# Kernel tuning notes

Hardware: AMD Instinct MI355X
Metric: run time of the kernel (lower is better)

The kernel has to match this reference:

```python
import jax, jax.numpy as jnp
import numpy as np

HEAD_SIZE = 128
NEG_INF = -1000000000.0

def setup_inputs() -> dict:
    key = jax.random.key(0)
    k1, k2, k3, k4 = jax.random.split(key, 4)
    B, T, C = 8, 2048, 1024
    x = jax.random.normal(k1, (B, T, C), dtype=jnp.float32)
    Wq = jax.random.normal(k2, (C, HEAD_SIZE), dtype=jnp.float32) * (1.0 / np.sqrt(C))
    Wk = jax.random.normal(k3, (C, HEAD_SIZE), dtype=jnp.float32) * (1.0 / np.sqrt(C))
    Wv = jax.random.normal(k4, (C, HEAD_SIZE), dtype=jnp.float32) * (1.0 / np.sqrt(C))
    return {"x": x, "Wq": Wq, "Wk": Wk, "Wv": Wv}

def reference(x, Wq, Wk, Wv):
    # x: [B, T, C]; projections: [B, T, H]
    T = x.shape[1]
    q = jnp.einsum('btc,ch->bth', x, Wq)
    k = jnp.einsum('btc,ch->bth', x, Wk)
    v = jnp.einsum('btc,ch->bth', x, Wv)
    scale = 1.0 / jnp.sqrt(jnp.float32(HEAD_SIZE))
    wei = jnp.einsum('bth,bsh->bts', q, k) * scale  # [B, T, T]
    causal = jnp.tril(jnp.ones((T, T), dtype=bool))
    wei = jnp.where(causal, wei, NEG_INF)
    wei = jax.nn.softmax(wei, axis=-1)
    # dropout is identity (deterministic=True)
    out = jnp.einsum('bts,bsh->bth', wei, v)  # [B, T, H]
    return out
```

## Files before the change

### kernel.cpp

```cpp
#include <hip/hip_runtime.h>
#include <hip/hip_bf16.h>
#include <stdint.h>

#define B_ 8
#define T_ 2048
#define C_ 1024
#define H_ 128
#define BT (B_*T_)
#define SCALE 0.08838834764831845f
#define SCL2  0.12751949703928947f
#define MFIX2 28.853900817779268f
#define CH 4
#define SLOTS_PB 140

typedef __attribute__((ext_vector_type(8))) short bf16x8;
typedef __attribute__((ext_vector_type(4))) float f32x4;

__device__ __forceinline__ ushort f2bf(float f) {
  union { float f; uint32_t u; } un; un.f = f;
  return (ushort)((un.u + 0x7fffu + ((un.u >> 16) & 1u)) >> 16);
}
__device__ __forceinline__ ushort f2bf_t(float f) {
  union { float f; uint32_t u; } un; un.f = f;
  return (ushort)(un.u >> 16);
}
__device__ __forceinline__ float bf2f(ushort h) {
  union { uint32_t u; float f; } un; un.u = ((uint32_t)h) << 16;
  return un.f;
}
__device__ __forceinline__ void gload16(const void* g, void* l) {
  __builtin_amdgcn_global_load_lds(
      (const __attribute__((address_space(1))) void*)g,
      (__attribute__((address_space(3))) void*)l, 16, 0, 0);
}

__global__ __launch_bounds__(256) void wtrans_kernel(
    const float* __restrict__ Wq, const float* __restrict__ Wk,
    const float* __restrict__ Wv, ushort* __restrict__ wt)
{
  const int tt = blockIdx.x * 256 + threadIdx.x;
  const int n = tt >> 6;
  const int k0 = (tt & 63) << 4;
  const float* W = (n < 128) ? Wq : (n < 256 ? Wk : Wv);
  const int h = n & 127;
  ushort tmp[16];
  #pragma unroll
  for (int j = 0; j < 16; ++j)
    tmp[j] = f2bf(W[(size_t)(k0 + j) * H_ + h]);
  *reinterpret_cast<bf16x8*>(&wt[(size_t)n * C_ + k0]) =
      *reinterpret_cast<bf16x8*>(&tmp[0]);
  *reinterpret_cast<bf16x8*>(&wt[(size_t)n * C_ + k0 + 8]) =
      *reinterpret_cast<bf16x8*>(&tmp[8]);
}

__global__ __launch_bounds__(256, 3) void proj_kernel(
    const float* __restrict__ x, const ushort* __restrict__ wt,
    ushort* __restrict__ qh, ushort* __restrict__ kh, ushort* __restrict__ vt)
{
  __shared__ __align__(16) ushort As[64][128];
  __shared__ __align__(16) ushort Bs[128][128];
  const int tid  = threadIdx.x;
  const int lane = tid & 63, wave = tid >> 6;
  const int l15  = lane & 15, l4 = lane >> 4;
  const int o  = (blockIdx.x & 7) * 96 + (blockIdx.x >> 3);
  const int mb = o / 3, nb = o - mb * 3;
  const int m0 = mb * 64, n0 = nb * 128;
  const int wr = wave >> 1, wc = wave & 1;

  f32x4 acc[2][4];
  #pragma unroll
  for (int i = 0; i < 2; ++i)
    #pragma unroll
    for (int j = 0; j < 4; ++j) acc[i][j] = f32x4{0.f, 0.f, 0.f, 0.f};

  for (int k0 = 0; k0 < C_; k0 += 128) {
    __syncthreads();
    #pragma unroll
    for (int j = 0; j < 8; ++j) {
      const int seg = wave * 8 + j;
      const int r = seg * 4 + (lane >> 4);
      const int c8 = lane & 15;
      const int c8g = (c8 & 8) | ((c8 & 7) ^ (r & 7));
      gload16(&wt[(size_t)(n0 + r) * C_ + k0 + c8g * 8], &Bs[seg * 4][0]);
    }
    float4 av[8];
    #pragma unroll
    for (int it = 0; it < 8; ++it) {
      const int f4 = it * 256 + tid;
      const int r = f4 >> 5, c4 = f4 & 31;
      av[it] = *reinterpret_cast<const float4*>(
          &x[(size_t)(m0 + r) * C_ + k0 + 4 * c4]);
    }
    #pragma unroll
    for (int it = 0; it < 8; ++it) {
      const int f4 = it * 256 + tid;
      const int r = f4 >> 5, c4 = f4 & 31;
      ushort4 pk;
      pk.x = f2bf(av[it].x); pk.y = f2bf(av[it].y);
      pk.z = f2bf(av[it].z); pk.w = f2bf(av[it].w);
      const int c = c4 >> 1;
      const int pos = (c & 8) | ((c & 7) ^ (r & 7));
      *reinterpret_cast<ushort4*>(&As[r][pos * 8 + (c4 & 1) * 4]) = pk;
    }
    __syncthreads();

    #pragma unroll
    for (int kv = 0; kv < 2; ++kv) {
      bf16x8 a[2][2], b[4][2];
      #pragma unroll
      for (int mi = 0; mi < 2; ++mi)
        #pragma unroll
        for (int kc = 0; kc < 2; ++kc) {
          const int row = wr * 32 + mi * 16 + l15;
          const int kc4 = (kv * 2 + kc) * 4 + l4;
          const int pos = (kc4 & 8) | ((kc4 & 7) ^ (row & 7));
          a[mi][kc] = *reinterpret_cast<const bf16x8*>(&As[row][pos * 8]);
        }
      #pragma unroll
      for (int ni = 0; ni < 4; ++ni)
        #pragma unroll
        for (int kc = 0; kc < 2; ++kc) {
          const int row = wc * 64 + ni * 16 + l15;
          const int kc4 = (kv * 2 + kc) * 4 + l4;
          const int pos = (kc4 & 8) | ((kc4 & 7) ^ (row & 7));
          b[ni][kc] = *reinterpret_cast<const bf16x8*>(&Bs[row][pos * 8]);
        }
      __builtin_amdgcn_s_setprio(1);
      if (nb != 2) {
        #pragma unroll
        for (int mi = 0; mi < 2; ++mi)
          #pragma unroll
          for (int ni = 0; ni < 4; ++ni)
            #pragma unroll
            for (int kc = 0; kc < 2; ++kc)
              acc[mi][ni] = __builtin_amdgcn_mfma_f32_16x16x32_bf16(
                  a[mi][kc], b[ni][kc], acc[mi][ni], 0, 0, 0);
      } else {
        #pragma unroll
        for (int mi = 0; mi < 2; ++mi)
          #pragma unroll
          for (int ni = 0; ni < 4; ++ni)
            #pragma unroll
            for (int kc = 0; kc < 2; ++kc)
              acc[mi][ni] = __builtin_amdgcn_mfma_f32_16x16x32_bf16(
                  b[ni][kc], a[mi][kc], acc[mi][ni], 0, 0, 0);
      }
      __builtin_amdgcn_s_setprio(0);
    }
  }

  if (nb != 2) {
    ushort* dst = (nb == 0) ? qh : kh;
    const float mul = (nb == 0) ? SCL2 : 1.0f;
    #pragma unroll
    for (int mi = 0; mi < 2; ++mi)
      #pragma unroll
      for (int ni = 0; ni < 4; ++ni)
        #pragma unroll
        for (int reg = 0; reg < 4; ++reg) {
          const int row = m0 + wr * 32 + mi * 16 + l4 * 4 + reg;
          const int col = wc * 64 + ni * 16 + l15;
          dst[(size_t)row * H_ + col] = f2bf(acc[mi][ni][reg] * mul);
        }
  } else {
    #pragma unroll
    for (int mi = 0; mi < 2; ++mi)
      #pragma unroll
      for (int ni = 0; ni < 4; ++ni)
        #pragma unroll
        for (int reg = 0; reg < 4; ++reg) {
          const int h = wc * 64 + ni * 16 + l4 * 4 + reg;
          const int gr = m0 + wr * 32 + mi * 16 + l15;
          const int b = gr >> 11, t = gr & 2047;
          vt[((size_t)b * H_ + h) * T_ + t] = f2bf(acc[mi][ni][reg]);
        }
  }
}

__global__ __launch_bounds__(256) void attn_kernel(
    const ushort* __restrict__ qh, const ushort* __restrict__ kh,
    const ushort* __restrict__ vt, ushort* __restrict__ pO,
    float* __restrict__ pl, float* __restrict__ out)
{
  __shared__ __align__(16) ushort Ks[64][128];
  __shared__ __align__(16) ushort Vs[128][64];
  __shared__ __align__(16) ushort Ps[4][16][64];
  const int tid  = threadIdx.x;
  const int lane = tid & 63, wave = tid >> 6;
  const int l15  = lane & 15, l4 = lane >> 4;
  const int o = (blockIdx.x & 7) * 144 + (blockIdx.x >> 3);
  const int b = o / 144;
  const int u = o - b * 144;
  int qi, ci, nchunk, u2 = 0;
  if (u < 4) { qi = u; ci = 0; nchunk = 1; }
  else {
    u2 = u - 4;
    int rem = u2, g = 1;
    while (rem >= 4 * (g + 1)) { rem -= 4 * (g + 1); ++g; }
    nchunk = g + 1;
    qi = 4 * g + rem / nchunk;
    ci = rem - (rem / nchunk) * nchunk;
  }
  const int q0 = qi * 64;
  const int kt0 = ci * CH;
  const int kt1 = min(qi + 1, kt0 + CH);
  const size_t mbase = (size_t)b * T_ + q0;
  const int swz = l15 & 7;

  const short one_bf = (short)0x3F80;
  const bf16x8 ones8 = {one_bf, one_bf, one_bf, one_bf,
                        one_bf, one_bf, one_bf, one_bf};

  bf16x8 qa[4];
  {
    const ushort* qrow = &qh[(mbase + wave * 16 + l15) * H_];
    #pragma unroll
    for (int kc = 0; kc < 4; ++kc)
      qa[kc] = *reinterpret_cast<const bf16x8*>(&qrow[kc * 32 + l4 * 8]);
  }

  f32x4 o_[8];
  #pragma unroll
  for (int i = 0; i < 8; ++i) o_[i] = f32x4{0.f, 0.f, 0.f, 0.f};
  float lrow[4] = {0.f, 0.f, 0.f, 0.f};

  for (int kt = kt0; kt < kt1; ++kt) {
    const int kv0 = kt * 64;
    __syncthreads();
    #pragma unroll
    for (int j = 0; j < 4; ++j) {
      const int r0 = wave * 16 + j * 4;
      const int r = r0 + (lane >> 4);
      const int c8 = lane & 15;
      const int c8g = (c8 & 8) | ((c8 & 7) ^ (r & 7));
      gload16(&kh[((size_t)b * T_ + kv0 + r) * H_ + c8g * 8], &Ks[r0][0]);
    }
    #pragma unroll
    for (int j = 0; j < 4; ++j) {
      const int r0 = wave * 32 + j * 8;
      const int r = r0 + (lane >> 3);
      const int c8g = (lane & 7) ^ (r & 7);
      gload16(&vt[((size_t)b * H_ + r) * T_ + kv0 + c8g * 8], &Vs[r0][0]);
    }
    __syncthreads();

    f32x4 s[4];
    __builtin_amdgcn_s_setprio(1);
    #pragma unroll
    for (int ct = 0; ct < 4; ++ct) {
      s[ct] = f32x4{0.f, 0.f, 0.f, 0.f};
      #pragma unroll
      for (int kc = 0; kc < 4; ++kc) {
        const int chunk = ((kc * 4 + l4) & 7) ^ swz;
        bf16x8 kb = *reinterpret_cast<const bf16x8*>(
            &Ks[ct * 16 + l15][(((kc * 4 + l4) & 8) | chunk) * 8]);
        s[ct] = __builtin_amdgcn_mfma_f32_16x16x32_bf16(qa[kc], kb, s[ct], 0, 0, 0);
      }
    }
    __builtin_amdgcn_s_setprio(0);

    const bool diag = (kv0 == q0);
    #pragma unroll
    for (int ct = 0; ct < 4; ++ct)
      #pragma unroll
      for (int reg = 0; reg < 4; ++reg) {
        float v = s[ct][reg];
        if (diag) {
          const int sg = kv0 + ct * 16 + l15;
          const int rg = q0 + wave * 16 + l4 * 4 + reg;
          if (sg > rg) v = -1e9f;
        }
        const float p = __builtin_amdgcn_exp2f(v - MFIX2);
        const int prow = l4 * 4 + reg;
        Ps[wave][prow][(ct * 16 + l15) ^ ((prow & 7) * 8)] = f2bf_t(p);
      }
    bf16x8 pa[2];
    #pragma unroll
    for (int kc = 0; kc < 2; ++kc)
      pa[kc] = *reinterpret_cast<const bf16x8*>(
          &Ps[wave][l15][((kc * 4 + l4) ^ swz) * 8]);
    __builtin_amdgcn_s_setprio(1);
    f32x4 sones = f32x4{0.f, 0.f, 0.f, 0.f};
    sones = __builtin_amdgcn_mfma_f32_16x16x32_bf16(pa[0], ones8, sones, 0, 0, 0);
    sones = __builtin_amdgcn_mfma_f32_16x16x32_bf16(pa[1], ones8, sones, 0, 0, 0);
    #pragma unroll
    for (int ct = 0; ct < 8; ++ct) {
      #pragma unroll
      for (int kc = 0; kc < 2; ++kc) {
        bf16x8 vb = *reinterpret_cast<const bf16x8*>(
            &Vs[ct * 16 + l15][((kc * 4 + l4) ^ swz) * 8]);
        o_[ct] = __builtin_amdgcn_mfma_f32_16x16x32_bf16(pa[kc], vb, o_[ct], 0, 0, 0);
      }
    }
    __builtin_amdgcn_s_setprio(0);
    #pragma unroll
    for (int reg = 0; reg < 4; ++reg) lrow[reg] += sones[reg];
  }

  if (nchunk == 1) {
    #pragma unroll
    for (int ct = 0; ct < 8; ++ct)
      #pragma unroll
      for (int reg = 0; reg < 4; ++reg) {
        const size_t row = mbase + wave * 16 + l4 * 4 + reg;
        out[row * H_ + ct * 16 + l15] = o_[ct][reg] / lrow[reg];
      }
  } else {
    const size_t slot = (size_t)b * SLOTS_PB + u2;
    ushort* po = pO + slot * 64 * 128;
    #pragma unroll
    for (int ct = 0; ct < 8; ++ct)
      #pragma unroll
      for (int reg = 0; reg < 4; ++reg) {
        const int row = wave * 16 + l4 * 4 + reg;
        po[(size_t)row * 128 + ct * 16 + l15] = f2bf(o_[ct][reg]);
      }
    #pragma unroll
    for (int reg = 0; reg < 4; ++reg) {
      if (l15 == 0) {
        const int row = wave * 16 + l4 * 4 + reg;
        pl[slot * 64 + row] = lrow[reg];
      }
    }
  }
}

__global__ __launch_bounds__(256) void combine_kernel(
    const ushort* __restrict__ pO, const float* __restrict__ pl,
    float* __restrict__ out)
{
  const int o = blockIdx.x;
  const int b = o / 28, qi = 4 + o % 28;
  const int G = qi >> 2;
  const int nc = G + 1;
  const int tid = threadIdx.x;
  const int row = tid >> 2, cg = tid & 3;
  const size_t slotbase =
      (size_t)b * SLOTS_PB + 2 * (G - 1) * (G + 2) + (qi & 3) * (G + 1);

  float L = 0.f;
  float acc[32];
  #pragma unroll
  for (int j = 0; j < 32; ++j) acc[j] = 0.f;
  for (int ci = 0; ci < nc; ++ci) {
    L += pl[(slotbase + ci) * 64 + row];
    const ushort* src = pO + (slotbase + ci) * 8192 + (size_t)row * 128 + cg * 32;
    #pragma unroll
    for (int j4 = 0; j4 < 4; ++j4) {
      bf16x8 v = *reinterpret_cast<const bf16x8*>(&src[j4 * 8]);
      #pragma unroll
      for (int j = 0; j < 8; ++j)
        acc[j4 * 8 + j] += bf2f((ushort)v[j]);
    }
  }
  const float inv = 1.f / L;
  float* dst = out + ((size_t)b * T_ + qi * 64 + row) * H_ + cg * 32;
  #pragma unroll
  for (int j4 = 0; j4 < 8; ++j4) {
    float4 w;
    w.x = acc[j4 * 4 + 0] * inv; w.y = acc[j4 * 4 + 1] * inv;
    w.z = acc[j4 * 4 + 2] * inv; w.w = acc[j4 * 4 + 3] * inv;
    *reinterpret_cast<float4*>(&dst[j4 * 4]) = w;
  }
}

extern "C" void kernel_launch(void* const* d_in, const int* in_sizes, int n_in,
                              void* d_out, int out_size, void* d_ws, size_t ws_size,
                              hipStream_t stream) {
  const float* x  = (const float*)d_in[0];
  const float* Wq = (const float*)d_in[1];
  const float* Wk = (const float*)d_in[2];
  const float* Wv = (const float*)d_in[3];
  float* out = (float*)d_out;
  ushort* qh = (ushort*)d_ws;
  ushort* kh = qh + (size_t)BT * H_;
  ushort* vt = kh + (size_t)BT * H_;
  ushort* wt = vt + (size_t)B_ * H_ * T_;
  ushort* pO = wt + (size_t)384 * C_;
  float*  pl = (float*)(pO + (size_t)B_ * SLOTS_PB * 64 * 128);
  wtrans_kernel<<<96, 256, 0, stream>>>(Wq, Wk, Wv, wt);
  proj_kernel<<<768, 256, 0, stream>>>(x, wt, qh, kh, vt);
  attn_kernel<<<1152, 256, 0, stream>>>(qh, kh, vt, pO, pl, out);
  combine_kernel<<<224, 256, 0, stream>>>(pO, pl, out);
}
```

Measured before the change: 66.93 us.

## Double-buffer projection GEMM LDS tiles with a 64-wide K step

```diff
diff --git a/kernel.cpp b/kernel.cpp
--- a/kernel.cpp
+++ b/kernel.cpp
@@ -57,8 +57,8 @@
     const float* __restrict__ x, const ushort* __restrict__ wt,
     ushort* __restrict__ qh, ushort* __restrict__ kh, ushort* __restrict__ vt)
 {
-  __shared__ __align__(16) ushort As[64][128];
-  __shared__ __align__(16) ushort Bs[128][128];
+  __shared__ __align__(16) ushort As[2][64][64];
+  __shared__ __align__(16) ushort Bs[2][128][64];
   const int tid  = threadIdx.x;
   const int lane = tid & 63, wave = tid >> 6;
   const int l15  = lane & 15, l4 = lane >> 4;
@@ -73,80 +73,88 @@
     #pragma unroll
     for (int j = 0; j < 4; ++j) acc[i][j] = f32x4{0.f, 0.f, 0.f, 0.f};
 
-  for (int k0 = 0; k0 < C_; k0 += 128) {
-    __syncthreads();
-    #pragma unroll
-    for (int j = 0; j < 8; ++j) {
-      const int seg = wave * 8 + j;
-      const int r = seg * 4 + (lane >> 4);
-      const int c8 = lane & 15;
-      const int c8g = (c8 & 8) | ((c8 & 7) ^ (r & 7));
-      gload16(&wt[(size_t)(n0 + r) * C_ + k0 + c8g * 8], &Bs[seg * 4][0]);
-    }
-    float4 av[8];
-    #pragma unroll
-    for (int it = 0; it < 8; ++it) {
+  float4 av[4];
+  auto b_dma = [&](int k0, int buf) {
+    #pragma unroll
+    for (int j = 0; j < 4; ++j) {
+      const int seg = wave * 4 + j;
+      const int r = seg * 8 + (lane >> 3);
+      const int c8g = (lane & 7) ^ (r & 7);
+      gload16(&wt[(size_t)(n0 + r) * C_ + k0 + c8g * 8], &Bs[buf][seg * 8][0]);
+    }
+  };
+  auto a_issue = [&](int k0) {
+    #pragma unroll
+    for (int it = 0; it < 4; ++it) {
       const int f4 = it * 256 + tid;
-      const int r = f4 >> 5, c4 = f4 & 31;
+      const int r = f4 >> 4, c4 = f4 & 15;
       av[it] = *reinterpret_cast<const float4*>(
           &x[(size_t)(m0 + r) * C_ + k0 + 4 * c4]);
     }
-    #pragma unroll
-    for (int it = 0; it < 8; ++it) {
+  };
+  auto a_write = [&](int buf) {
+    #pragma unroll
+    for (int it = 0; it < 4; ++it) {
       const int f4 = it * 256 + tid;
-      const int r = f4 >> 5, c4 = f4 & 31;
+      const int r = f4 >> 4, c4 = f4 & 15;
       ushort4 pk;
       pk.x = f2bf(av[it].x); pk.y = f2bf(av[it].y);
       pk.z = f2bf(av[it].z); pk.w = f2bf(av[it].w);
-      const int c = c4 >> 1;
-      const int pos = (c & 8) | ((c & 7) ^ (r & 7));
-      *reinterpret_cast<ushort4*>(&As[r][pos * 8 + (c4 & 1) * 4]) = pk;
-    }
-    __syncthreads();
-
-    #pragma unroll
-    for (int kv = 0; kv < 2; ++kv) {
-      bf16x8 a[2][2], b[4][2];
+      const int ch = (c4 >> 1) ^ (r & 7);
+      *reinterpret_cast<ushort4*>(&As[buf][r][ch * 8 + (c4 & 1) * 4]) = pk;
+    }
+  };
+
+  b_dma(0, 0);
+  a_issue(0);
+  a_write(0);
+  __syncthreads();
+
+  for (int t = 0; t < 16; ++t) {
+    const int cur = t & 1, nxt = cur ^ 1;
+    if (t < 15) { b_dma((t + 1) * 64, nxt); a_issue((t + 1) * 64); }
+
+    bf16x8 a[2][2], b[4][2];
+    #pragma unroll
+    for (int mi = 0; mi < 2; ++mi)
+      #pragma unroll
+      for (int kc = 0; kc < 2; ++kc) {
+        const int row = wr * 32 + mi * 16 + l15;
+        const int ch = (kc * 4 + l4) ^ (row & 7);
+        a[mi][kc] = *reinterpret_cast<const bf16x8*>(&As[cur][row][ch * 8]);
+      }
+    #pragma unroll
+    for (int ni = 0; ni < 4; ++ni)
+      #pragma unroll
+      for (int kc = 0; kc < 2; ++kc) {
+        const int row = wc * 64 + ni * 16 + l15;
+        const int ch = (kc * 4 + l4) ^ (row & 7);
+        b[ni][kc] = *reinterpret_cast<const bf16x8*>(&Bs[cur][row][ch * 8]);
+      }
+    __builtin_amdgcn_s_setprio(1);
+    if (nb != 2) {
       #pragma unroll
       for (int mi = 0; mi < 2; ++mi)
         #pragma unroll
-        for (int kc = 0; kc < 2; ++kc) {
-          const int row = wr * 32 + mi * 16 + l15;
-          const int kc4 = (kv * 2 + kc) * 4 + l4;
-          const int pos = (kc4 & 8) | ((kc4 & 7) ^ (row & 7));
-          a[mi][kc] = *reinterpret_cast<const bf16x8*>(&As[row][pos * 8]);
-        }
-      #pragma unroll
-      for (int ni = 0; ni < 4; ++ni)
+        for (int ni = 0; ni < 4; ++ni)
+          #pragma unroll
+          for (int kc = 0; kc < 2; ++kc)
+            acc[mi][ni] = __builtin_amdgcn_mfma_f32_16x16x32_bf16(
+                a[mi][kc], b[ni][kc], acc[mi][ni], 0, 0, 0);
+    } else {
+      #pragma unroll
+      for (int mi = 0; mi < 2; ++mi)
         #pragma unroll
-        for (int kc = 0; kc < 2; ++kc) {
-          const int row = wc * 64 + ni * 16 + l15;
-          const int kc4 = (kv * 2 + kc) * 4 + l4;
-          const int pos = (kc4 & 8) | ((kc4 & 7) ^ (row & 7));
-          b[ni][kc] = *reinterpret_cast<const bf16x8*>(&Bs[row][pos * 8]);
-        }
-      __builtin_amdgcn_s_setprio(1);
-      if (nb != 2) {
-        #pragma unroll
-        for (int mi = 0; mi < 2; ++mi)
+        for (int ni = 0; ni < 4; ++ni)
           #pragma unroll
-          for (int ni = 0; ni < 4; ++ni)
-            #pragma unroll
-            for (int kc = 0; kc < 2; ++kc)
-              acc[mi][ni] = __builtin_amdgcn_mfma_f32_16x16x32_bf16(
-                  a[mi][kc], b[ni][kc], acc[mi][ni], 0, 0, 0);
-      } else {
-        #pragma unroll
-        for (int mi = 0; mi < 2; ++mi)
-          #pragma unroll
-          for (int ni = 0; ni < 4; ++ni)
-            #pragma unroll
-            for (int kc = 0; kc < 2; ++kc)
-              acc[mi][ni] = __builtin_amdgcn_mfma_f32_16x16x32_bf16(
-                  b[ni][kc], a[mi][kc], acc[mi][ni], 0, 0, 0);
-      }
-      __builtin_amdgcn_s_setprio(0);
-    }
+          for (int kc = 0; kc < 2; ++kc)
+            acc[mi][ni] = __builtin_amdgcn_mfma_f32_16x16x32_bf16(
+                b[ni][kc], a[mi][kc], acc[mi][ni], 0, 0, 0);
+    }
+    __builtin_amdgcn_s_setprio(0);
+
+    if (t < 15) a_write(nxt);
+    __syncthreads();
   }
 
   if (nb != 2) {
```

Result: slower. 69.15 us (+3.3%).
